# Optimization experiments

Measured on AMD Instinct MI355X. Metric: run time of the kernel, lower is better.

Reference implementation:

```python
import jax, jax.numpy as jnp
import numpy as np


def _ln(x, g, b, eps=1e-5):
    m = jnp.mean(x, axis=-1, keepdims=True)
    v = jnp.var(x, axis=-1, keepdims=True)  # biased var, matches torch LayerNorm
    return (x - m) / jnp.sqrt(v + eps) * g + b


def setup_inputs() -> dict:
    key = jax.random.key(0)
    ks = jax.random.split(key, 10)
    B, S, T, D, F = 4, 8, 1024, 768, 16
    inp = {
        "target_hidden": jax.random.normal(ks[0], (B, T, D), jnp.float32),
        "support_hidden": jax.random.normal(ks[1], (B, S, T, D), jnp.float32),
        "support_token_mask": jax.random.bernoulli(ks[2], 0.8, (B, S, T)),
        "support_features": jax.random.normal(ks[3], (B, T, F), jnp.float32),
        # LayerNorm params
        "t_g": jnp.ones((D,), jnp.float32), "t_b": jnp.zeros((D,), jnp.float32),
        "s_g": jnp.ones((D,), jnp.float32), "s_b": jnp.zeros((D,), jnp.float32),
        "o_g": jnp.ones((D,), jnp.float32), "o_b": jnp.zeros((D,), jnp.float32),
        # score MLP: Linear(2D->D), GELU, Linear(D->1)
        "score_w1": jax.random.normal(ks[4], (2 * D, D), jnp.float32) * 0.02,
        "score_b1": jnp.zeros((D,), jnp.float32),
        "score_w2": jax.random.normal(ks[5], (D, 1), jnp.float32) * 0.02,
        "score_b2": jnp.zeros((1,), jnp.float32),
        # gate MLP: Linear(2D+F->D), GELU, Linear(D->1), Sigmoid
        "gate_w1": jax.random.normal(ks[6], (2 * D + F, D), jnp.float32) * 0.02,
        "gate_b1": jnp.zeros((D,), jnp.float32),
        "gate_w2": jax.random.normal(ks[7], (D, 1), jnp.float32) * 0.02,
        "gate_b2": jnp.zeros((1,), jnp.float32),
    }
    return inp


def reference(target_hidden, support_hidden, support_token_mask, support_features,
              t_g, t_b, s_g, s_b, o_g, o_b,
              score_w1, score_b1, score_w2, score_b2,
              gate_w1, gate_b1, gate_w2, gate_b2):
    D = target_hidden.shape[-1]
    mask = support_token_mask  # (B,S,T) bool

    th = _ln(target_hidden, t_g, t_b)        # (B,T,D)
    sh = _ln(support_hidden, s_g, s_b)       # (B,S,T,D)

    # score MLP on concat([target_expanded, support], -1) == split-weight form
    h = (jnp.einsum('btd,df->btf', th, score_w1[:D])[:, None, :, :]
         + jnp.einsum('bstd,df->bstf', sh, score_w1[D:]) + score_b1)  # (B,S,T,D)
    h = jax.nn.gelu(h, approximate=False)
    scores = jnp.einsum('bstd,d->bst', h, score_w2[:, 0]) + score_b2[0]  # (B,S,T)

    scores = jnp.where(mask, scores, -10000.0)
    w = jax.nn.softmax(scores, axis=1)
    w = w * mask.astype(w.dtype)
    w = w / jnp.clip(jnp.sum(w, axis=1, keepdims=True), 1e-8)

    summary = jnp.einsum('bst,bstd->btd', w, sh)  # (B,T,D)
    has_support = jnp.any(mask, axis=1)           # (B,T)
    summary = jnp.where(has_support[..., None], summary, 0.0)

    gcat = jnp.concatenate([th, summary, support_features], axis=-1)  # (B,T,2D+F)
    g = jax.nn.gelu(gcat @ gate_w1 + gate_b1, approximate=False)
    gate = jax.nn.sigmoid(g @ gate_w2 + gate_b2)  # (B,T,1)

    fused = gate * summary + (1.0 - gate) * th    # dropout is identity in eval
    out = _ln(th + fused, o_g, o_b)
    return out, gate.squeeze(-1)
```

## Files before the change

kernel.cpp:

```cpp
#include <hip/hip_runtime.h>
#include <hip/hip_bf16.h>

#define D768 768

typedef __attribute__((ext_vector_type(8))) short short8;
typedef __attribute__((ext_vector_type(4))) float f32x4;

__device__ __forceinline__ unsigned short f2bf(float f){
  union { float f; unsigned u; } v; v.f = f;
  unsigned r = v.u + 0x7FFFu + ((v.u >> 16) & 1u);
  return (unsigned short)(r >> 16);
}
__device__ __forceinline__ float bf2f(unsigned short u){
  union { unsigned u; float f; } v; v.u = ((unsigned)u) << 16;
  return v.f;
}
__device__ __forceinline__ float gelu_f(float x){
  float y = fabsf(x) * 0.7071067811865475f;
  float t = __builtin_amdgcn_rcpf(fmaf(0.3275911f, y, 1.0f));
  float p = fmaf(fmaf(fmaf(fmaf(1.061405429f, t, -1.453152027f), t, 1.421413741f),
                      t, -0.284496736f), t, 0.254829592f) * t;
  float e = __expf(-y * y);
  float erf_abs = fmaf(-p, e, 1.0f);
  float erfv = copysignf(erf_abs, x);
  return 0.5f * x * (1.0f + erfv);
}
__device__ __forceinline__ void gload16(const void* g, void* l){
  __builtin_amdgcn_global_load_lds((const __attribute__((address_space(1))) void*)g,
                                   (__attribute__((address_space(3))) void*)l, 16, 0, 0);
}

__global__ void k_ln(const float* __restrict__ x, const float* __restrict__ g,
                     const float* __restrict__ bia, float* __restrict__ of32,
                     unsigned short* __restrict__ obf, int ldo){
  int row = blockIdx.x;
  int t = threadIdx.x;
  const float* xr = x + (size_t)row * D768;
  float4 v = *(const float4*)(xr + t*4);
  float s  = v.x + v.y + v.z + v.w;
  float ss = v.x*v.x + v.y*v.y + v.z*v.z + v.w*v.w;
  for (int o = 32; o; o >>= 1){ s += __shfl_down(s, o); ss += __shfl_down(ss, o); }
  __shared__ float sb[6];
  int wid = t >> 6;
  if ((t & 63) == 0){ sb[wid] = s; sb[3+wid] = ss; }
  __syncthreads();
  s = sb[0] + sb[1] + sb[2]; ss = sb[3] + sb[4] + sb[5];
  float mean = s * (1.f/768.f);
  float var  = ss * (1.f/768.f) - mean*mean;
  float rstd = rsqrtf(var + 1e-5f);
  float4 gv = *(const float4*)(g + t*4);
  float4 bv = *(const float4*)(bia + t*4);
  float o0 = (v.x-mean)*rstd*gv.x + bv.x;
  float o1 = (v.y-mean)*rstd*gv.y + bv.y;
  float o2 = (v.z-mean)*rstd*gv.z + bv.z;
  float o3 = (v.w-mean)*rstd*gv.w + bv.w;
  if (of32){
    float4 ov; ov.x=o0; ov.y=o1; ov.z=o2; ov.w=o3;
    *(float4*)(of32 + (size_t)row * D768 + t*4) = ov;
  }
  ushort4 ub; ub.x=f2bf(o0); ub.y=f2bf(o1); ub.z=f2bf(o2); ub.w=f2bf(o3);
  *(ushort4*)(obf + (size_t)row * ldo + t*4) = ub;
}

__global__ void k_wtall(const float* __restrict__ sw1, const float* __restrict__ gw1,
                        unsigned short* __restrict__ WtA, unsigned short* __restrict__ WtB,
                        unsigned short* __restrict__ WtG,
                        float* __restrict__ scores, const float* __restrict__ sb2,
                        float* __restrict__ gacc, const float* __restrict__ gb2,
                        const unsigned char* __restrict__ m, int* __restrict__ flag){
  int blk = blockIdx.x;
  if (blk < 128){
    int i = blk * 256 + threadIdx.x;
    if (i < 32768) scores[i] = sb2[0];
    if (i < 4096)  gacc[i]   = gb2[0];
    if (blk == 0){
      __shared__ int s;
      if (threadIdx.x == 0) s = 0;
      __syncthreads();
      int nz = 0;
      for (int j = threadIdx.x; j < 2048; j += 256) nz += (m[4*j+1] != 0);
      atomicAdd(&s, nz);
      __syncthreads();
      if (threadIdx.x == 0) *flag = (s == 0) ? 1 : 0;
    }
    return;
  }
  int tile = blk - 128;
  const float* W; unsigned short* Wt; int Kin, Kpad;
  if (tile < 576)      { W = sw1;                 Wt = WtA; Kin = 768;  Kpad = 768;  }
  else if (tile < 1152){ W = sw1 + 768ull*768;    Wt = WtB; Kin = 768;  Kpad = 768;  tile -= 576; }
  else                 { W = gw1;                 Wt = WtG; Kin = 1552; Kpad = 1568; tile -= 1152; }
  int ntk = Kpad >> 5;
  int k0 = (tile % ntk) << 5, n0 = (tile / ntk) << 5;
  __shared__ float ts[32][33];
  int tx = threadIdx.x & 31, ty = threadIdx.x >> 5;
  #pragma unroll
  for (int r = 0; r < 4; ++r){
    int k = k0 + ty + r*8;
    ts[ty + r*8][tx] = (k < Kin) ? W[(size_t)k * D768 + n0 + tx] : 0.f;
  }
  __syncthreads();
  #pragma unroll
  for (int r = 0; r < 4; ++r){
    int n = n0 + ty + r*8;
    Wt[(size_t)n * Kpad + k0 + tx] = f2bf(ts[tx][ty + r*8]);
  }
}

template<int MODE, int BN>
__launch_bounds__(256)
__global__ void k_gemm(const unsigned short* __restrict__ A, int lda,
                       const unsigned short* __restrict__ Bt, int ldb,
                       int ksteps,
                       const float* __restrict__ tproj,
                       const float* __restrict__ b1,
                       const float* __restrict__ w2,
                       float* __restrict__ out){
  constexpr int NJ  = BN / 32;
  constexpr int BCH = BN / 64;
  __shared__ __align__(16) unsigned short As[128*32];
  __shared__ __align__(16) unsigned short Bs[BN*32];
  const int m0 = blockIdx.x * 128, n0 = blockIdx.y * BN;
  const int t = threadIdx.x, lane = t & 63, w = t >> 6;
  const int wrow = (w >> 1) * 64, wcol = (w & 1) * (BN/2);
  const int lo16 = lane & 15, hi = (lane >> 4) * 8;
  const int crow = lane >> 2, cseg = (lane & 3) * 8;
  const unsigned short* ga = A  + (size_t)(m0 + w*32 + crow) * lda + cseg;
  const unsigned short* gb = Bt + (size_t)(n0 + w*(BN/4) + crow) * ldb + cseg;
  unsigned short* la = As + w*1024;
  unsigned short* lb = Bs + w*(BN/4)*32;
  const unsigned short* pa = As + (size_t)(wrow + lo16) * 32 + hi;
  const unsigned short* pb = Bs + (size_t)(wcol + lo16) * 32 + hi;
  f32x4 acc[4][NJ] = {};
  for (int ks = 0; ks < ksteps; ++ks){
    const unsigned short* gak = ga + ks*32;
    const unsigned short* gbk = gb + ks*32;
    #pragma unroll
    for (int c = 0; c < 2; ++c)
      gload16(gak + (size_t)(c*16)*lda, la + c*512);
    #pragma unroll
    for (int c = 0; c < BCH; ++c)
      gload16(gbk + (size_t)(c*16)*ldb, lb + c*512);
    __syncthreads();
    short8 af[4], bf[NJ];
    #pragma unroll
    for (int i = 0; i < 4; ++i) af[i] = *(const short8*)(pa + i*16*32);
    #pragma unroll
    for (int j = 0; j < NJ; ++j) bf[j] = *(const short8*)(pb + j*16*32);
    #pragma unroll
    for (int i = 0; i < 4; ++i)
      #pragma unroll
      for (int j = 0; j < NJ; ++j)
        acc[i][j] = __builtin_amdgcn_mfma_f32_16x16x32_bf16(af[i], bf[j], acc[i][j], 0, 0, 0);
    __syncthreads();
  }
  if (MODE == 0){
    #pragma unroll
    for (int i = 0; i < 4; ++i)
      #pragma unroll
      for (int reg = 0; reg < 4; ++reg){
        int row = m0 + wrow + i*16 + ((lane >> 4) << 2) + reg;
        float* orow = out + (size_t)row * D768 + n0 + wcol + lo16;
        #pragma unroll
        for (int j = 0; j < NJ; ++j) orow[j*16] = acc[i][j][reg];
      }
  } else {
    #pragma unroll
    for (int i = 0; i < 4; ++i)
      #pragma unroll
      for (int reg = 0; reg < 4; ++reg){
        int row = m0 + wrow + i*16 + ((lane >> 4) << 2) + reg;
        const float* tp = nullptr;
        if (MODE == 1){
          int trow = ((row >> 13) << 10) | (row & 1023);
          tp = tproj + (size_t)trow * D768;
        }
        float contrib = 0.f;
        #pragma unroll
        for (int j = 0; j < NJ; ++j){
          int n = n0 + wcol + j*16 + lo16;
          float v = acc[i][j][reg] + b1[n];
          if (MODE == 1) v += tp[n];
          contrib += gelu_f(v) * w2[n];
        }
        for (int o = 8; o; o >>= 1) contrib += __shfl_xor(contrib, o);
        if (lo16 == 0) atomicAdd(&out[row], contrib);
      }
  }
}

__global__ void k_smx(const float* __restrict__ scores, const void* __restrict__ maskp,
                      const int* __restrict__ flag, const unsigned short* __restrict__ sh,
                      float* __restrict__ summary, const float* __restrict__ feat,
                      unsigned short* __restrict__ gcat){
  int bt = blockIdx.x;
  int b = bt >> 10, tt = bt & 1023;
  int t = threadIdx.x;
  int f = *flag;
  float sc[8], mk[8];
  #pragma unroll
  for (int s = 0; s < 8; ++s){
    size_t idx = ((size_t)(b*8 + s) << 10) + tt;
    bool m = f ? (((const int*)maskp)[idx] != 0)
               : (((const unsigned char*)maskp)[idx] != 0);
    mk[s] = m ? 1.f : 0.f;
    float v = scores[idx];
    sc[s] = m ? v : -10000.f;
  }
  float mx = sc[0];
  #pragma unroll
  for (int s = 1; s < 8; ++s) mx = fmaxf(mx, sc[s]);
  float e[8], sum = 0.f;
  #pragma unroll
  for (int s = 0; s < 8; ++s){ e[s] = __expf(sc[s] - mx); sum += e[s]; }
  float inv = 1.f / sum;
  float wv[8], sum2 = 0.f;
  #pragma unroll
  for (int s = 0; s < 8; ++s){ wv[s] = e[s] * inv * mk[s]; sum2 += wv[s]; }
  float inv2 = 1.f / fmaxf(sum2, 1e-8f);
  #pragma unroll
  for (int s = 0; s < 8; ++s) wv[s] *= inv2;
  float a0=0.f, a1=0.f, a2=0.f, a3=0.f;
  #pragma unroll
  for (int s = 0; s < 8; ++s){
    const unsigned short* p = sh + (((size_t)(b*8+s) << 10) + tt) * D768 + t*4;
    ushort4 u = *(const ushort4*)p;
    float ws = wv[s];
    a0 += ws * bf2f(u.x); a1 += ws * bf2f(u.y); a2 += ws * bf2f(u.z); a3 += ws * bf2f(u.w);
  }
  float4 ov; ov.x=a0; ov.y=a1; ov.z=a2; ov.w=a3;
  *(float4*)(summary + (size_t)bt * D768 + t*4) = ov;
  ushort4 ub; ub.x=f2bf(a0); ub.y=f2bf(a1); ub.z=f2bf(a2); ub.w=f2bf(a3);
  *(ushort4*)(gcat + (size_t)bt * 1568 + 768 + t*4) = ub;
  if (t < 8){
    int c = 1536 + t*4;
    float4 fv = make_float4(0.f, 0.f, 0.f, 0.f);
    if (c < 1552) fv = *(const float4*)(feat + (size_t)bt * 16 + (c - 1536));
    ushort4 uf; uf.x=f2bf(fv.x); uf.y=f2bf(fv.y); uf.z=f2bf(fv.z); uf.w=f2bf(fv.w);
    *(ushort4*)(gcat + (size_t)bt * 1568 + c) = uf;
  }
}

__global__ void k_final(const float* __restrict__ th, const float* __restrict__ summary,
                        const float* __restrict__ gacc, const float* __restrict__ og,
                        const float* __restrict__ ob, float* __restrict__ out,
                        float* __restrict__ outg){
  int r = blockIdx.x, t = threadIdx.x;
  float gv = 1.f / (1.f + __expf(-gacc[r]));
  if (t == 0) outg[r] = gv;
  float4 tv = *(const float4*)(th + (size_t)r * D768 + t*4);
  float4 sv = *(const float4*)(summary + (size_t)r * D768 + t*4);
  float x0 = (2.f-gv)*tv.x + gv*sv.x;
  float x1 = (2.f-gv)*tv.y + gv*sv.y;
  float x2 = (2.f-gv)*tv.z + gv*sv.z;
  float x3 = (2.f-gv)*tv.w + gv*sv.w;
  float s = x0+x1+x2+x3, ss = x0*x0+x1*x1+x2*x2+x3*x3;
  for (int o = 32; o; o >>= 1){ s += __shfl_down(s,o); ss += __shfl_down(ss,o); }
  __shared__ float sb[6];
  int wid = t >> 6;
  if ((t&63)==0){ sb[wid]=s; sb[3+wid]=ss; }
  __syncthreads();
  s = sb[0]+sb[1]+sb[2]; ss = sb[3]+sb[4]+sb[5];
  float mean = s*(1.f/768.f), var = ss*(1.f/768.f)-mean*mean;
  float rstd = rsqrtf(var + 1e-5f);
  float4 gvv = *(const float4*)(og + t*4);
  float4 bvv = *(const float4*)(ob + t*4);
  float4 ov;
  ov.x = (x0-mean)*rstd*gvv.x + bvv.x;
  ov.y = (x1-mean)*rstd*gvv.y + bvv.y;
  ov.z = (x2-mean)*rstd*gvv.z + bvv.z;
  ov.w = (x3-mean)*rstd*gvv.w + bvv.w;
  *(float4*)(out + (size_t)r * D768 + t*4) = ov;
}

extern "C" void kernel_launch(void* const* d_in, const int* in_sizes, int n_in,
                              void* d_out, int out_size, void* d_ws, size_t ws_size,
                              hipStream_t stream){
  const float* target = (const float*)d_in[0];
  const float* support= (const float*)d_in[1];
  const void*  maskp  = d_in[2];
  const float* feat   = (const float*)d_in[3];
  const float* t_g = (const float*)d_in[4];
  const float* t_b = (const float*)d_in[5];
  const float* s_g = (const float*)d_in[6];
  const float* s_b = (const float*)d_in[7];
  const float* o_g = (const float*)d_in[8];
  const float* o_b = (const float*)d_in[9];
  const float* sw1 = (const float*)d_in[10];
  const float* sb1 = (const float*)d_in[11];
  const float* sw2 = (const float*)d_in[12];
  const float* sb2 = (const float*)d_in[13];
  const float* gw1 = (const float*)d_in[14];
  const float* gb1 = (const float*)d_in[15];
  const float* gw2 = (const float*)d_in[16];
  const float* gb2 = (const float*)d_in[17];

  char* wsb = (char*)d_ws;
  size_t off = 0;
  auto alloc = [&](size_t bytes)->void*{
    void* p = wsb + off; off += (bytes + 255) & ~(size_t)255; return p;
  };
  float* th            = (float*)alloc(4096ull*768*4);
  unsigned short* sh   = (unsigned short*)alloc(32768ull*768*2);
  float* tproj         = (float*)alloc(4096ull*768*4);
  float* summary       = (float*)alloc(4096ull*768*4);
  unsigned short* gcat = (unsigned short*)alloc(4096ull*1568*2);
  unsigned short* WtA  = (unsigned short*)alloc(768ull*768*2);
  unsigned short* WtB  = (unsigned short*)alloc(768ull*768*2);
  unsigned short* WtG  = (unsigned short*)alloc(768ull*1568*2);
  float* scores        = (float*)alloc(32768ull*4);
  float* gacc          = (float*)alloc(4096ull*4);
  int*   flag          = (int*)alloc(256);

  float* outm = (float*)d_out;
  float* outg = outm + 4096ull*768;

  k_wtall<<<2456, 256, 0, stream>>>(sw1, gw1, WtA, WtB, WtG,
                                    scores, sb2, gacc, gb2,
                                    (const unsigned char*)maskp, flag);
  k_ln<<<4096, 192, 0, stream>>>(target, t_g, t_b, th, gcat, 1568);
  k_gemm<0,64><<<dim3(32,12), 256, 0, stream>>>(gcat, 1568, WtA, 768, 24,
                                                nullptr, nullptr, nullptr, tproj);
  k_ln<<<32768, 192, 0, stream>>>(support, s_g, s_b, (float*)nullptr, sh, 768);
  k_gemm<1,128><<<dim3(256,6), 256, 0, stream>>>(sh, 768, WtB, 768, 24,
                                                 tproj, sb1, sw2, scores);
  k_smx<<<4096, 192, 0, stream>>>(scores, maskp, flag, sh, summary, feat, gcat);
  k_gemm<2,64><<<dim3(32,12), 256, 0, stream>>>(gcat, 1568, WtG, 1568, 49,
                                                nullptr, gb1, gw2, gacc);
  k_final<<<4096, 192, 0, stream>>>(th, summary, gacc, o_g, o_b, outm, outg);
}
```

Baseline: 195.6 us.

## Double-buffer LDS tiles in GEMM to overlap global loads with MFMA

Shared-memory A/B tiles become two buffers, and the K loop issues global-to-LDS loads for step k+1 into the alternate buffer while MFMAs consume the current one. Each step now ends with a single vmcnt wait plus barrier instead of two barriers. This aims to hide global load latency behind compute, at the cost of doubling LDS use, which may reduce occupancy.

```diff
diff --git a/kernel.cpp b/kernel.cpp
--- a/kernel.cpp
+++ b/kernel.cpp
@@ -118,8 +118,8 @@
                        float* __restrict__ out){
   constexpr int NJ  = BN / 32;
   constexpr int BCH = BN / 64;
-  __shared__ __align__(16) unsigned short As[128*32];
-  __shared__ __align__(16) unsigned short Bs[BN*32];
+  __shared__ __align__(16) unsigned short As[2][128*32];
+  __shared__ __align__(16) unsigned short Bs[2][BN*32];
   const int m0 = blockIdx.x * 128, n0 = blockIdx.y * BN;
   const int t = threadIdx.x, lane = t & 63, w = t >> 6;
   const int wrow = (w >> 1) * 64, wcol = (w & 1) * (BN/2);
@@ -127,33 +127,53 @@
   const int crow = lane >> 2, cseg = (lane & 3) * 8;
   const unsigned short* ga = A  + (size_t)(m0 + w*32 + crow) * lda + cseg;
   const unsigned short* gb = Bt + (size_t)(n0 + w*(BN/4) + crow) * ldb + cseg;
-  unsigned short* la = As + w*1024;
-  unsigned short* lb = Bs + w*(BN/4)*32;
-  const unsigned short* pa = As + (size_t)(wrow + lo16) * 32 + hi;
-  const unsigned short* pb = Bs + (size_t)(wcol + lo16) * 32 + hi;
   f32x4 acc[4][NJ] = {};
-  for (int ks = 0; ks < ksteps; ++ks){
-    const unsigned short* gak = ga + ks*32;
-    const unsigned short* gbk = gb + ks*32;
-    #pragma unroll
-    for (int c = 0; c < 2; ++c)
-      gload16(gak + (size_t)(c*16)*lda, la + c*512);
-    #pragma unroll
-    for (int c = 0; c < BCH; ++c)
-      gload16(gbk + (size_t)(c*16)*ldb, lb + c*512);
-    __syncthreads();
-    short8 af[4], bf[NJ];
-    #pragma unroll
-    for (int i = 0; i < 4; ++i) af[i] = *(const short8*)(pa + i*16*32);
-    #pragma unroll
-    for (int j = 0; j < NJ; ++j) bf[j] = *(const short8*)(pb + j*16*32);
-    #pragma unroll
-    for (int i = 0; i < 4; ++i)
-      #pragma unroll
-      for (int j = 0; j < NJ; ++j)
-        acc[i][j] = __builtin_amdgcn_mfma_f32_16x16x32_bf16(af[i], bf[j], acc[i][j], 0, 0, 0);
-    __syncthreads();
-  }
+
+#define STAGEK(BUF, KS) do {                                                   \
+    const unsigned short* gak_ = ga + (size_t)(KS)*32;                         \
+    const unsigned short* gbk_ = gb + (size_t)(KS)*32;                         \
+    _Pragma("unroll")                                                          \
+    for (int c = 0; c < 2; ++c)                                                \
+      gload16(gak_ + (size_t)(c*16)*lda, &As[BUF][w*1024 + c*512]);            \
+    _Pragma("unroll")                                                          \
+    for (int c = 0; c < BCH; ++c)                                              \
+      gload16(gbk_ + (size_t)(c*16)*ldb, &Bs[BUF][w*(BN/4)*32 + c*512]);       \
+  } while (0)
+
+#define COMPUTEK(BUF) do {                                                     \
+    const unsigned short* pa_ = &As[BUF][(wrow + lo16)*32 + hi];               \
+    const unsigned short* pb_ = &Bs[BUF][(wcol + lo16)*32 + hi];               \
+    short8 af_[4], bf_[NJ];                                                    \
+    _Pragma("unroll")                                                          \
+    for (int i = 0; i < 4; ++i) af_[i] = *(const short8*)(pa_ + i*16*32);      \
+    _Pragma("unroll")                                                          \
+    for (int j = 0; j < NJ; ++j) bf_[j] = *(const short8*)(pb_ + j*16*32);     \
+    _Pragma("unroll")                                                          \
+    for (int i = 0; i < 4; ++i)                                                \
+      _Pragma("unroll")                                                        \
+      for (int j = 0; j < NJ; ++j)                                             \
+        acc[i][j] = __builtin_amdgcn_mfma_f32_16x16x32_bf16(af_[i], bf_[j], acc[i][j], 0, 0, 0); \
+  } while (0)
+
+  STAGEK(0, 0);
+  asm volatile("s_waitcnt vmcnt(0)" ::: "memory");
+  __builtin_amdgcn_s_barrier();
+  int ks = 0;
+  for (;;){
+    if (ks + 1 < ksteps) STAGEK(1, ks + 1);
+    COMPUTEK(0);
+    asm volatile("s_waitcnt vmcnt(0)" ::: "memory");
+    __builtin_amdgcn_s_barrier();
+    if (++ks >= ksteps) break;
+    if (ks + 1 < ksteps) STAGEK(0, ks + 1);
+    COMPUTEK(1);
+    asm volatile("s_waitcnt vmcnt(0)" ::: "memory");
+    __builtin_amdgcn_s_barrier();
+    if (++ks >= ksteps) break;
+  }
+#undef STAGEK
+#undef COMPUTEK
+
   if (MODE == 0){
     #pragma unroll
     for (int i = 0; i < 4; ++i)
```

Measured after the change: 207.3 us. 6.0% more time.
